# Kernel optimization log

Measured on AMD Instinct MI355X. Metric: run time of the kernel, lower is better.

Reference implementation:

```python
import jax, jax.numpy as jnp
import numpy as np

SIZE = 4096      # number of 2D images stacked on channel axis
IMG = 64         # image_size
N_MULTS = 4      # len(mul_approx_func_arr)


def setup_inputs() -> dict:
    key = jax.random.key(0)
    k1, k2, k3 = jax.random.split(key, 3)
    inp = jax.random.normal(k1, (1, SIZE, IMG, IMG), dtype=jnp.float32)
    # Laplacian-sharpen init, tiled per multiplier index (as in __init__)
    base = jnp.asarray([-1., -1., -1., -1., 8., -1., -1., -1., -1.], dtype=jnp.float32) / 8.0
    weight = jnp.tile(base, (N_MULTS, 1)) + 0.01 * jax.random.normal(k2, (N_MULTS, 9), dtype=jnp.float32)
    weight_factor = jnp.full((N_MULTS, 1), 8.0, dtype=jnp.float32) + jax.random.normal(k3, (N_MULTS, 1), dtype=jnp.float32)
    return {"input": inp, "weight": weight, "weight_factor": weight_factor}


def reference(input, weight, weight_factor):
    # input: [1, C, H, W]; weight: [n, 9]; weight_factor: [n, 1]
    n = weight.shape[0]
    # hardtanh clamps (the in-place .data clamp makes these equivalent to clip)
    w = jnp.clip(weight, -1.0, 1.0) * jnp.clip(weight_factor, 1.0, 255.0)  # [n, 9]
    kernels = w.reshape(n, 1, 3, 3)

    # Unfold + per-element multiply + sum over the 9 taps == depthwise 3x3 conv
    # with the SAME kernel on every channel. Put channels on the batch axis so a
    # single conv evaluates all n mult indices at once. (mul_wrapper approximate
    # multiplier modeled as exact multiply.)
    x = input[0][:, None]  # [C, 1, H, W]
    conv = jax.lax.conv_general_dilated(
        x, kernels, window_strides=(1, 1), padding=((1, 1), (1, 1)),
        dimension_numbers=("NCHW", "OIHW", "NCHW"))  # [C, n, H, W]
    result = jnp.transpose(conv, (1, 0, 2, 3))[:, None]  # [n, 1, C, H, W]

    # approx_sharp: div = max(result)/128 per mult index; approx_division snaps
    # the divisor to the nearest power of two (round(log2(div))).
    div = jnp.max(result, axis=(1, 2, 3, 4), keepdims=True) / 128.0  # [n,1,1,1,1]
    shift = jnp.round(jnp.log2(div))
    shifted = result / jnp.exp2(shift)
    out = jnp.where(div > 0, shifted, result)
    # output[ii][0] = input + shifted result -> [n, 1, C, H, W]
    return input[None] + out
```

## Files before the change

kernel.cpp:

```cpp
#include <hip/hip_runtime.h>
#include <math.h>

#define NCH 4096
#define IMG 64
#define HW  (IMG * IMG)
#define NM  4
#define TPAD 65

#define WS_FINAL (NCH * NM)

__device__ __forceinline__ void load_weights(const float* __restrict__ wgt,
                                             const float* __restrict__ wf,
                                             float k[NM][9]) {
#pragma unroll
    for (int n = 0; n < NM; ++n) {
        float f = fminf(fmaxf(wf[n], 1.0f), 255.0f);
#pragma unroll
        for (int j = 0; j < 9; ++j) {
            float w = fminf(fmaxf(wgt[n * 9 + j], -1.0f), 1.0f);
            k[n][j] = w * f;
        }
    }
}

__device__ __forceinline__ void stage_tile(const float* __restrict__ img,
                                           float* tile, int t) {
    const float4* img4 = (const float4*)img;
#pragma unroll
    for (int i = 0; i < 4; ++i) {
        int idx = t + i * 256;
        float4 v = img4[idx];
        int p = idx * 4;
        int h = p >> 6;
        int w = p & 63;
        float* dst = &tile[h * TPAD + w];
        dst[0] = v.x; dst[1] = v.y; dst[2] = v.z; dst[3] = v.w;
    }
}

__device__ __forceinline__ void load_taps(const float* tile, int h, int w0,
                                          float tap[3][6]) {
#pragma unroll
    for (int dy = -1; dy <= 1; ++dy) {
        int hh = h + dy;
        bool okh = (hh >= 0) && (hh < IMG);
#pragma unroll
        for (int dx = -1; dx <= 4; ++dx) {
            int ww = w0 + dx;
            bool ok = okh && (ww >= 0) && (ww < IMG);
            int idx = ok ? (hh * TPAD + ww) : 0;
            float v = tile[idx];
            tap[dy + 1][dx + 1] = ok ? v : 0.0f;
        }
    }
}

__global__ __launch_bounds__(256) void conv_max_kernel(
        const float* __restrict__ in, const float* __restrict__ wgt,
        const float* __restrict__ wf, float* __restrict__ ws) {
    __shared__ float tile[IMG * TPAD];
    __shared__ float red[4][NM];
    const int c = blockIdx.x;
    const int t = threadIdx.x;
    const float* img = in + (size_t)c * HW;

    stage_tile(img, tile, t);
    float k[NM][9];
    load_weights(wgt, wf, k);
    __syncthreads();

    float m[NM] = {-INFINITY, -INFINITY, -INFINITY, -INFINITY};
#pragma unroll
    for (int g = 0; g < 4; ++g) {
        int pix = (t + g * 256) * 4;
        int h = pix >> 6;
        int w0 = pix & 63;
        float tap[3][6];
        load_taps(tile, h, w0, tap);
#pragma unroll
        for (int i = 0; i < 4; ++i) {
#pragma unroll
            for (int n = 0; n < NM; ++n) {
                float acc = 0.0f;
#pragma unroll
                for (int dy = 0; dy < 3; ++dy)
#pragma unroll
                    for (int dx = 0; dx < 3; ++dx)
                        acc = fmaf(k[n][dy * 3 + dx], tap[dy][dx + i], acc);
                m[n] = fmaxf(m[n], acc);
            }
        }
    }

#pragma unroll
    for (int off = 32; off >= 1; off >>= 1)
#pragma unroll
        for (int n = 0; n < NM; ++n)
            m[n] = fmaxf(m[n], __shfl_down(m[n], off, 64));

    const int wave = t >> 6, lane = t & 63;
    if (lane == 0)
#pragma unroll
        for (int n = 0; n < NM; ++n) red[wave][n] = m[n];
    __syncthreads();
    if (t == 0) {
        float4 v;
        v.x = fmaxf(fmaxf(red[0][0], red[1][0]), fmaxf(red[2][0], red[3][0]));
        v.y = fmaxf(fmaxf(red[0][1], red[1][1]), fmaxf(red[2][1], red[3][1]));
        v.z = fmaxf(fmaxf(red[0][2], red[1][2]), fmaxf(red[2][2], red[3][2]));
        v.w = fmaxf(fmaxf(red[0][3], red[1][3]), fmaxf(red[2][3], red[3][3]));
        *(float4*)(ws + (size_t)c * NM) = v;
    }
}

__global__ __launch_bounds__(256) void reduce_max_kernel(float* __restrict__ ws) {
    __shared__ float red[4][NM];
    const int t = threadIdx.x;
    const float4* p4 = (const float4*)ws;
    float4 m = {-INFINITY, -INFINITY, -INFINITY, -INFINITY};
#pragma unroll
    for (int i = 0; i < NCH / 256; ++i) {
        float4 v = p4[t + i * 256];
        m.x = fmaxf(m.x, v.x); m.y = fmaxf(m.y, v.y);
        m.z = fmaxf(m.z, v.z); m.w = fmaxf(m.w, v.w);
    }
#pragma unroll
    for (int off = 32; off >= 1; off >>= 1) {
        m.x = fmaxf(m.x, __shfl_down(m.x, off, 64));
        m.y = fmaxf(m.y, __shfl_down(m.y, off, 64));
        m.z = fmaxf(m.z, __shfl_down(m.z, off, 64));
        m.w = fmaxf(m.w, __shfl_down(m.w, off, 64));
    }
    const int wave = t >> 6, lane = t & 63;
    if (lane == 0) {
        red[wave][0] = m.x; red[wave][1] = m.y;
        red[wave][2] = m.z; red[wave][3] = m.w;
    }
    __syncthreads();
    if (t == 0) {
        float4 v;
        v.x = fmaxf(fmaxf(red[0][0], red[1][0]), fmaxf(red[2][0], red[3][0]));
        v.y = fmaxf(fmaxf(red[0][1], red[1][1]), fmaxf(red[2][1], red[3][1]));
        v.z = fmaxf(fmaxf(red[0][2], red[1][2]), fmaxf(red[2][2], red[3][2]));
        v.w = fmaxf(fmaxf(red[0][3], red[1][3]), fmaxf(red[2][3], red[3][3]));
        *(float4*)(ws + WS_FINAL) = v;
    }
}

__global__ __launch_bounds__(256) void conv_out_kernel(
        const float* __restrict__ in, const float* __restrict__ wgt,
        const float* __restrict__ wf, const float* __restrict__ mx,
        float* __restrict__ out) {
    __shared__ float tile[IMG * TPAD];
    const int c = blockIdx.x;
    const int t = threadIdx.x;
    const float* img = in + (size_t)c * HW;

    stage_tile(img, tile, t);
    float k[NM][9];
    load_weights(wgt, wf, k);

    float inv[NM];
#pragma unroll
    for (int n = 0; n < NM; ++n) {
        float m = mx[n];
        float div = m * (1.0f / 128.0f);
        if (div > 0.0f) {
            float shift = rintf(log2f(div));
            inv[n] = exp2f(-shift);
        } else {
            inv[n] = 1.0f;
        }
    }
    __syncthreads();

#pragma unroll
    for (int g = 0; g < 4; ++g) {
        int pix = (t + g * 256) * 4;
        int h = pix >> 6;
        int w0 = pix & 63;
        float tap[3][6];
        load_taps(tile, h, w0, tap);
        float4 o[NM];
#pragma unroll
        for (int n = 0; n < NM; ++n) {
            float* op = (float*)&o[n];
#pragma unroll
            for (int i = 0; i < 4; ++i) {
                float acc = 0.0f;
#pragma unroll
                for (int dy = 0; dy < 3; ++dy)
#pragma unroll
                    for (int dx = 0; dx < 3; ++dx)
                        acc = fmaf(k[n][dy * 3 + dx], tap[dy][dx + i], acc);
                op[i] = tap[1][i + 1] + acc * inv[n];
            }
        }
#pragma unroll
        for (int n = 0; n < NM; ++n) {
            size_t off = ((size_t)n * NCH + c) * HW + pix;
            *(float4*)(out + off) = o[n];
        }
    }
}

extern "C" void kernel_launch(void* const* d_in, const int* in_sizes, int n_in,
                              void* d_out, int out_size, void* d_ws, size_t ws_size,
                              hipStream_t stream) {
    const float* in  = (const float*)d_in[0];
    const float* wgt = (const float*)d_in[1];
    const float* wf  = (const float*)d_in[2];
    float* out = (float*)d_out;
    float* ws  = (float*)d_ws;

    conv_max_kernel<<<dim3(NCH), dim3(256), 0, stream>>>(in, wgt, wf, ws);
    reduce_max_kernel<<<dim3(1), dim3(256), 0, stream>>>(ws);
    conv_out_kernel<<<dim3(NCH), dim3(256), 0, stream>>>(in, wgt, wf, ws + WS_FINAL, out);
}
```

Measured before the change: 330.9 us.

## Fuse final max reduction into output kernel, pad tile, use nontemporal stores

Removes the single-block reduce kernel by having each output block redundantly reduce the 1024 per-block maxima itself. The max pass now processes four channels per block, so it writes fewer partial maxima. The shared tile gains a zero border, so tap loads need no bounds checks. Output writes become nontemporal stores, which avoids polluting the cache with the large output. The cost is redundant reduction work in every output block and one fewer launch between the two passes.

After: 317.1 us. 4.2% less time.

```diff
diff --git a/kernel.cpp b/kernel.cpp
--- a/kernel.cpp
+++ b/kernel.cpp
@@ -5,9 +5,16 @@
 #define IMG 64
 #define HW  (IMG * IMG)
 #define NM  4
-#define TPAD 65
-
-#define WS_FINAL (NCH * NM)
+
+typedef float nfloat4 __attribute__((ext_vector_type(4)));
+
+#define TP    69
+#define TROWS 66
+#define TILE_FLOATS (TROWS * TP)
+
+#define GRID1 1024
+#define CPB1  (NCH / GRID1)
+
 
 __device__ __forceinline__ void load_weights(const float* __restrict__ wgt,
                                              const float* __restrict__ wf,
@@ -20,6 +27,18 @@
             float w = fminf(fmaxf(wgt[n * 9 + j], -1.0f), 1.0f);
             k[n][j] = w * f;
         }
+    }
+}
+
+__device__ __forceinline__ void zero_border(float* tile, int t) {
+#pragma unroll
+    for (int b = t; b < 260; b += 256) {
+        int r, cidx;
+        if (b < 66)       { r = 0;            cidx = b; }
+        else if (b < 132) { r = 65;           cidx = b - 66; }
+        else if (b < 196) { r = b - 132 + 1;  cidx = 0; }
+        else              { r = b - 196 + 1;  cidx = 65; }
+        tile[r * TP + cidx] = 0.0f;
     }
 }
 
@@ -33,7 +52,7 @@
         int p = idx * 4;
         int h = p >> 6;
         int w = p & 63;
-        float* dst = &tile[h * TPAD + w];
+        float* dst = &tile[(h + 1) * TP + (w + 1)];
         dst[0] = v.x; dst[1] = v.y; dst[2] = v.z; dst[3] = v.w;
     }
 }
@@ -41,35 +60,135 @@
 __device__ __forceinline__ void load_taps(const float* tile, int h, int w0,
                                           float tap[3][6]) {
 #pragma unroll
-    for (int dy = -1; dy <= 1; ++dy) {
-        int hh = h + dy;
-        bool okh = (hh >= 0) && (hh < IMG);
-#pragma unroll
-        for (int dx = -1; dx <= 4; ++dx) {
-            int ww = w0 + dx;
-            bool ok = okh && (ww >= 0) && (ww < IMG);
-            int idx = ok ? (hh * TPAD + ww) : 0;
-            float v = tile[idx];
-            tap[dy + 1][dx + 1] = ok ? v : 0.0f;
-        }
+    for (int r = 0; r < 3; ++r) {
+        const float* row = &tile[(h + r) * TP + w0];
+#pragma unroll
+        for (int cdx = 0; cdx < 6; ++cdx)
+            tap[r][cdx] = row[cdx];
     }
 }
 
 __global__ __launch_bounds__(256) void conv_max_kernel(
         const float* __restrict__ in, const float* __restrict__ wgt,
         const float* __restrict__ wf, float* __restrict__ ws) {
-    __shared__ float tile[IMG * TPAD];
+    __shared__ float tile[TILE_FLOATS];
+    __shared__ float red[4][NM];
+    const int t = threadIdx.x;
+
+    float k[NM][9];
+    load_weights(wgt, wf, k);
+    zero_border(tile, t);
+
+    float m[NM] = {-INFINITY, -INFINITY, -INFINITY, -INFINITY};
+
+#pragma unroll
+    for (int cc = 0; cc < CPB1; ++cc) {
+        const int c = blockIdx.x * CPB1 + cc;
+        const float* img = in + (size_t)c * HW;
+        __syncthreads();
+        stage_tile(img, tile, t);
+        __syncthreads();
+
+#pragma unroll
+        for (int g = 0; g < 4; ++g) {
+            int pix = (t + g * 256) * 4;
+            int h = pix >> 6;
+            int w0 = pix & 63;
+            float tap[3][6];
+            load_taps(tile, h, w0, tap);
+#pragma unroll
+            for (int i = 0; i < 4; ++i) {
+#pragma unroll
+                for (int n = 0; n < NM; ++n) {
+                    float acc = 0.0f;
+#pragma unroll
+                    for (int dy = 0; dy < 3; ++dy)
+#pragma unroll
+                        for (int dx = 0; dx < 3; ++dx)
+                            acc = fmaf(k[n][dy * 3 + dx], tap[dy][dx + i], acc);
+                    m[n] = fmaxf(m[n], acc);
+                }
+            }
+        }
+    }
+
+#pragma unroll
+    for (int off = 32; off >= 1; off >>= 1)
+#pragma unroll
+        for (int n = 0; n < NM; ++n)
+            m[n] = fmaxf(m[n], __shfl_down(m[n], off, 64));
+
+    const int wave = t >> 6, lane = t & 63;
+    if (lane == 0)
+#pragma unroll
+        for (int n = 0; n < NM; ++n) red[wave][n] = m[n];
+    __syncthreads();
+    if (t == 0) {
+        float4 v;
+        v.x = fmaxf(fmaxf(red[0][0], red[1][0]), fmaxf(red[2][0], red[3][0]));
+        v.y = fmaxf(fmaxf(red[0][1], red[1][1]), fmaxf(red[2][1], red[3][1]));
+        v.z = fmaxf(fmaxf(red[0][2], red[1][2]), fmaxf(red[2][2], red[3][2]));
+        v.w = fmaxf(fmaxf(red[0][3], red[1][3]), fmaxf(red[2][3], red[3][3]));
+        *(float4*)(ws + (size_t)blockIdx.x * NM) = v;
+    }
+}
+
+__global__ __launch_bounds__(256) void conv_out_kernel(
+        const float* __restrict__ in, const float* __restrict__ wgt,
+        const float* __restrict__ wf, const float* __restrict__ ws,
+        float* __restrict__ out) {
+    __shared__ float tile[TILE_FLOATS];
     __shared__ float red[4][NM];
     const int c = blockIdx.x;
     const int t = threadIdx.x;
     const float* img = in + (size_t)c * HW;
 
-    stage_tile(img, tile, t);
+    const float4* p4 = (const float4*)ws;
+    float4 mm = {-INFINITY, -INFINITY, -INFINITY, -INFINITY};
+#pragma unroll
+    for (int i = 0; i < GRID1 / 256; ++i) {
+        float4 v = p4[t + i * 256];
+        mm.x = fmaxf(mm.x, v.x); mm.y = fmaxf(mm.y, v.y);
+        mm.z = fmaxf(mm.z, v.z); mm.w = fmaxf(mm.w, v.w);
+    }
+#pragma unroll
+    for (int off = 32; off >= 1; off >>= 1) {
+        mm.x = fmaxf(mm.x, __shfl_down(mm.x, off, 64));
+        mm.y = fmaxf(mm.y, __shfl_down(mm.y, off, 64));
+        mm.z = fmaxf(mm.z, __shfl_down(mm.z, off, 64));
+        mm.w = fmaxf(mm.w, __shfl_down(mm.w, off, 64));
+    }
+    const int wave = t >> 6, lane = t & 63;
+    if (lane == 0) {
+        red[wave][0] = mm.x; red[wave][1] = mm.y;
+        red[wave][2] = mm.z; red[wave][3] = mm.w;
+    }
+    __syncthreads();
+    float fin[NM];
+#pragma unroll
+    for (int n = 0; n < NM; ++n)
+        fin[n] = fmaxf(fmaxf(red[0][n], red[1][n]), fmaxf(red[2][n], red[3][n]));
+
+    float inv[NM];
+#pragma unroll
+    for (int n = 0; n < NM; ++n) {
+        float div = fin[n] * (1.0f / 128.0f);
+        if (div > 0.0f) {
+            float shift = rintf(log2f(div));
+            inv[n] = exp2f(-shift);
+        } else {
+            inv[n] = 1.0f;
+        }
+    }
+
     float k[NM][9];
     load_weights(wgt, wf, k);
-    __syncthreads();
-
-    float m[NM] = {-INFINITY, -INFINITY, -INFINITY, -INFINITY};
+
+    __syncthreads();
+    zero_border(tile, t);
+    stage_tile(img, tile, t);
+    __syncthreads();
+
 #pragma unroll
     for (int g = 0; g < 4; ++g) {
         int pix = (t + g * 256) * 4;
@@ -78,128 +197,20 @@
         float tap[3][6];
         load_taps(tile, h, w0, tap);
 #pragma unroll
-        for (int i = 0; i < 4; ++i) {
-#pragma unroll
-            for (int n = 0; n < NM; ++n) {
+        for (int n = 0; n < NM; ++n) {
+            nfloat4 o;
+#pragma unroll
+            for (int i = 0; i < 4; ++i) {
                 float acc = 0.0f;
 #pragma unroll
                 for (int dy = 0; dy < 3; ++dy)
 #pragma unroll
                     for (int dx = 0; dx < 3; ++dx)
                         acc = fmaf(k[n][dy * 3 + dx], tap[dy][dx + i], acc);
-                m[n] = fmaxf(m[n], acc);
+                o[i] = tap[1][i + 1] + acc * inv[n];
             }
-        }
-    }
-
-#pragma unroll
-    for (int off = 32; off >= 1; off >>= 1)
-#pragma unroll
-        for (int n = 0; n < NM; ++n)
-            m[n] = fmaxf(m[n], __shfl_down(m[n], off, 64));
-
-    const int wave = t >> 6, lane = t & 63;
-    if (lane == 0)
-#pragma unroll
-        for (int n = 0; n < NM; ++n) red[wave][n] = m[n];
-    __syncthreads();
-    if (t == 0) {
-        float4 v;
-        v.x = fmaxf(fmaxf(red[0][0], red[1][0]), fmaxf(red[2][0], red[3][0]));
-        v.y = fmaxf(fmaxf(red[0][1], red[1][1]), fmaxf(red[2][1], red[3][1]));
-        v.z = fmaxf(fmaxf(red[0][2], red[1][2]), fmaxf(red[2][2], red[3][2]));
-        v.w = fmaxf(fmaxf(red[0][3], red[1][3]), fmaxf(red[2][3], red[3][3]));
-        *(float4*)(ws + (size_t)c * NM) = v;
-    }
-}
-
-__global__ __launch_bounds__(256) void reduce_max_kernel(float* __restrict__ ws) {
-    __shared__ float red[4][NM];
-    const int t = threadIdx.x;
-    const float4* p4 = (const float4*)ws;
-    float4 m = {-INFINITY, -INFINITY, -INFINITY, -INFINITY};
-#pragma unroll
-    for (int i = 0; i < NCH / 256; ++i) {
-        float4 v = p4[t + i * 256];
-        m.x = fmaxf(m.x, v.x); m.y = fmaxf(m.y, v.y);
-        m.z = fmaxf(m.z, v.z); m.w = fmaxf(m.w, v.w);
-    }
-#pragma unroll
-    for (int off = 32; off >= 1; off >>= 1) {
-        m.x = fmaxf(m.x, __shfl_down(m.x, off, 64));
-        m.y = fmaxf(m.y, __shfl_down(m.y, off, 64));
-        m.z = fmaxf(m.z, __shfl_down(m.z, off, 64));
-        m.w = fmaxf(m.w, __shfl_down(m.w, off, 64));
-    }
-    const int wave = t >> 6, lane = t & 63;
-    if (lane == 0) {
-        red[wave][0] = m.x; red[wave][1] = m.y;
-        red[wave][2] = m.z; red[wave][3] = m.w;
-    }
-    __syncthreads();
-    if (t == 0) {
-        float4 v;
-        v.x = fmaxf(fmaxf(red[0][0], red[1][0]), fmaxf(red[2][0], red[3][0]));
-        v.y = fmaxf(fmaxf(red[0][1], red[1][1]), fmaxf(red[2][1], red[3][1]));
-        v.z = fmaxf(fmaxf(red[0][2], red[1][2]), fmaxf(red[2][2], red[3][2]));
-        v.w = fmaxf(fmaxf(red[0][3], red[1][3]), fmaxf(red[2][3], red[3][3]));
-        *(float4*)(ws + WS_FINAL) = v;
-    }
-}
-
-__global__ __launch_bounds__(256) void conv_out_kernel(
-        const float* __restrict__ in, const float* __restrict__ wgt,
-        const float* __restrict__ wf, const float* __restrict__ mx,
-        float* __restrict__ out) {
-    __shared__ float tile[IMG * TPAD];
-    const int c = blockIdx.x;
-    const int t = threadIdx.x;
-    const float* img = in + (size_t)c * HW;
-
-    stage_tile(img, tile, t);
-    float k[NM][9];
-    load_weights(wgt, wf, k);
-
-    float inv[NM];
-#pragma unroll
-    for (int n = 0; n < NM; ++n) {
-        float m = mx[n];
-        float div = m * (1.0f / 128.0f);
-        if (div > 0.0f) {
-            float shift = rintf(log2f(div));
-            inv[n] = exp2f(-shift);
-        } else {
-            inv[n] = 1.0f;
-        }
-    }
-    __syncthreads();
-
-#pragma unroll
-    for (int g = 0; g < 4; ++g) {
-        int pix = (t + g * 256) * 4;
-        int h = pix >> 6;
-        int w0 = pix & 63;
-        float tap[3][6];
-        load_taps(tile, h, w0, tap);
-        float4 o[NM];
-#pragma unroll
-        for (int n = 0; n < NM; ++n) {
-            float* op = (float*)&o[n];
-#pragma unroll
-            for (int i = 0; i < 4; ++i) {
-                float acc = 0.0f;
-#pragma unroll
-                for (int dy = 0; dy < 3; ++dy)
-#pragma unroll
-                    for (int dx = 0; dx < 3; ++dx)
-                        acc = fmaf(k[n][dy * 3 + dx], tap[dy][dx + i], acc);
-                op[i] = tap[1][i + 1] + acc * inv[n];
-            }
-        }
-#pragma unroll
-        for (int n = 0; n < NM; ++n) {
             size_t off = ((size_t)n * NCH + c) * HW + pix;
-            *(float4*)(out + off) = o[n];
+            __builtin_nontemporal_store(o, (nfloat4*)(out + off));
         }
     }
 }
@@ -213,7 +224,6 @@
     float* out = (float*)d_out;
     float* ws  = (float*)d_ws;
 
-    conv_max_kernel<<<dim3(NCH), dim3(256), 0, stream>>>(in, wgt, wf, ws);
-    reduce_max_kernel<<<dim3(1), dim3(256), 0, stream>>>(ws);
-    conv_out_kernel<<<dim3(NCH), dim3(256), 0, stream>>>(in, wgt, wf, ws + WS_FINAL, out);
-}
+    conv_max_kernel<<<dim3(GRID1), dim3(256), 0, stream>>>(in, wgt, wf, ws);
+    conv_out_kernel<<<dim3(NCH), dim3(256), 0, stream>>>(in, wgt, wf, ws, out);
+}
```
